# Kernel optimization log

Measured on AMD Instinct MI355X. Metric: run time of the kernel, lower is better.

## Reference

```python
import jax, jax.numpy as jnp
import numpy as np

# --- hyperparameters (from MambaBlock init) ---
DIM = 256          # d_model per window
STEP = 128         # int(dim * hop), hop = 0.5
N_MAMBA = 2
D_STATE = 16
D_CONV = 4
EXPAND = 4
D_INNER = EXPAND * DIM          # 1024
DT_RANK = -(-DIM // 16)         # ceil(d_model/16) = 16
EPS = 1e-5
B_SZ = 4
T_LEN = 131072


def setup_inputs() -> dict:
    key = jax.random.key(0)
    ks = jax.random.split(key, 8)
    s = 0.02
    x = jax.random.normal(ks[0], (B_SZ, T_LEN), dtype=jnp.float32)
    in_proj_w = jax.random.normal(ks[1], (N_MAMBA, 2 * D_INNER, DIM), dtype=jnp.float32) * s
    conv_w = jax.random.normal(ks[2], (N_MAMBA, D_INNER, 1, D_CONV), dtype=jnp.float32) * 0.1
    conv_b = jnp.zeros((N_MAMBA, D_INNER), dtype=jnp.float32)
    x_proj_w = jax.random.normal(ks[3], (N_MAMBA, DT_RANK + 2 * D_STATE, D_INNER), dtype=jnp.float32) * s
    dt_std = DT_RANK ** -0.5
    dt_proj_w = jax.random.uniform(ks[4], (N_MAMBA, D_INNER, DT_RANK), minval=-dt_std, maxval=dt_std, dtype=jnp.float32)
    # dt bias: inverse-softplus of dt ~ LogUniform[1e-3, 0.1] (mamba_ssm init)
    dt = jnp.exp(jax.random.uniform(ks[5], (N_MAMBA, D_INNER), dtype=jnp.float32)
                 * (np.log(0.1) - np.log(1e-3)) + np.log(1e-3))
    dt_proj_b = dt + jnp.log(-jnp.expm1(-dt))
    A_log = jnp.log(jnp.broadcast_to(jnp.arange(1, D_STATE + 1, dtype=jnp.float32),
                                     (N_MAMBA, D_INNER, D_STATE)))
    D_param = jnp.ones((N_MAMBA, D_INNER), dtype=jnp.float32)
    out_proj_w = jax.random.normal(ks[6], (N_MAMBA, DIM, D_INNER), dtype=jnp.float32) * s
    norm_w = jnp.ones((N_MAMBA, DIM), dtype=jnp.float32)
    return dict(x=x, in_proj_w=in_proj_w, conv_w=conv_w, conv_b=conv_b,
                x_proj_w=x_proj_w, dt_proj_w=dt_proj_w, dt_proj_b=dt_proj_b,
                A_log=A_log, D_param=D_param, out_proj_w=out_proj_w, norm_w=norm_w)


def _rmsnorm(x, w):
    return x * jax.lax.rsqrt(jnp.mean(x * x, axis=-1, keepdims=True) + EPS) * w


def _selective_scan(u, delta, A, Bm, Cm, Dp):
    # u, delta: [B, L, Di]; A: [Di, N]; Bm, Cm: [B, L, N]; Dp: [Di]
    def step(h, inp):
        u_t, d_t, B_t, C_t = inp                       # [B,Di],[B,Di],[B,N],[B,N]
        dA = jnp.exp(d_t[:, :, None] * A)              # [B,Di,N]
        h = dA * h + (d_t * u_t)[:, :, None] * B_t[:, None, :]
        y_t = jnp.einsum('bdn,bn->bd', h, C_t)
        return h, y_t
    h0 = jnp.zeros((u.shape[0], u.shape[2], A.shape[1]), u.dtype)
    xs = (u.transpose(1, 0, 2), delta.transpose(1, 0, 2),
          Bm.transpose(1, 0, 2), Cm.transpose(1, 0, 2))
    _, ys = jax.lax.scan(step, h0, xs)                 # ys: [L, B, Di]
    return ys.transpose(1, 0, 2) + u * Dp


def _mamba(x, in_w, cw, cb, xp_w, dt_w, dt_b, A_log, Dp, out_w):
    # x: [B, L, d_model]
    xz = jnp.einsum('bld,ed->ble', x, in_w)            # [B, L, 2*Di]
    xc, z = jnp.split(xz, 2, axis=-1)
    # causal depthwise conv (torch pads d_conv-1 both sides then truncates to L)
    xc = xc.transpose(0, 2, 1)                         # [B, Di, L]
    xc = jax.lax.conv_general_dilated(xc, cw, window_strides=(1,),
                                      padding=[(D_CONV - 1, 0)],
                                      feature_group_count=D_INNER,
                                      dimension_numbers=('NCH', 'OIH', 'NCH'))
    xc = jax.nn.silu(xc + cb[None, :, None]).transpose(0, 2, 1)  # [B, L, Di]
    x_dbl = jnp.einsum('bld,ed->ble', xc, xp_w)        # [B, L, dt_rank + 2N]
    dt = x_dbl[..., :DT_RANK]
    Bm = x_dbl[..., DT_RANK:DT_RANK + D_STATE]
    Cm = x_dbl[..., DT_RANK + D_STATE:]
    delta = jax.nn.softplus(jnp.einsum('blr,dr->bld', dt, dt_w) + dt_b)
    A = -jnp.exp(A_log)                                # [Di, N]
    y = _selective_scan(xc, delta, A, Bm, Cm, Dp)
    y = y * jax.nn.silu(z)
    return jnp.einsum('bld,ed->ble', y, out_w)         # [B, L, d_model]


def _forward(x, in_proj_w, conv_w, conv_b, x_proj_w, dt_proj_w, dt_proj_b,
             A_log, D_param, out_proj_w, norm_w):
    B, T = x.shape
    L = (T - DIM) // STEP + 1
    idx = jnp.arange(L)[:, None] * STEP + jnp.arange(DIM)[None, :]  # [L, DIM]
    h = x[:, idx]                                      # unfold -> [B, L, DIM]
    res = None
    for i in range(N_MAMBA):
        res = h + res if res is not None else h        # Block residual chaining
        hn = _rmsnorm(res, norm_w[i])
        h = _mamba(hn, in_proj_w[i], conv_w[i], conv_b[i], x_proj_w[i],
                   dt_proj_w[i], dt_proj_b[i], A_log[i], D_param[i], out_proj_w[i])
    r = h + res
    # hop < 1: triangular window, then fold (overlap-add)
    half = DIM // 2
    win = jnp.concatenate([jnp.linspace(0.0, 1.0, half), jnp.linspace(1.0, 0.0, half)])
    r = r * win
    folded = jnp.zeros_like(x).at[:, idx].add(r)       # F.fold overlap-add
    return folded + x


def reference(x, in_proj_w, conv_w, conv_b, x_proj_w, dt_proj_w, dt_proj_b,
              A_log, D_param, out_proj_w, norm_w):
    return _forward(x, in_proj_w, conv_w, conv_b, x_proj_w, dt_proj_w, dt_proj_b,
                    A_log, D_param, out_proj_w, norm_w)
```

## Files before the change

kernel.cpp:

```cpp
#include <hip/hip_runtime.h>
#include <cmath>

#define DIMC   256
#define L_WIN  1023
#define M_VALID 4092
#define M_PAD  4096
#define DI     1024
#define TLEN   131072
#define SEG    32
#define NSEG   32
#define CBT    8

typedef __bf16 bf16x8 __attribute__((ext_vector_type(8)));
typedef __bf16 bf16x4 __attribute__((ext_vector_type(4)));
typedef float  f32x4  __attribute__((ext_vector_type(4)));

__device__ __forceinline__ float sigmoidf_(float x){ return 1.f/(1.f + __expf(-x)); }
__device__ __forceinline__ float softplusf_(float v){ return fmaxf(v,0.f) + log1pf(__expf(-fabsf(v))); }

template<int CTRL>
__device__ __forceinline__ float dpp_add(float x){
  int v = __builtin_amdgcn_update_dpp(0, __builtin_bit_cast(int, x), CTRL, 0xF, 0xF, true);
  return x + __builtin_bit_cast(float, v);
}

__global__ __launch_bounds__(256) void init_kernel(const float* __restrict__ x, float* __restrict__ res,
    const float* __restrict__ a, __bf16* __restrict__ da, int na,
    const float* __restrict__ b, __bf16* __restrict__ db, int nb,
    const float* __restrict__ c, __bf16* __restrict__ dc, int nc)
{
  if (blockIdx.x < M_PAD){
    int m = blockIdx.x, j = threadIdx.x;
    float v = 0.f;
    if (m < M_VALID){
      int bb = m / L_WIN, l = m - bb*L_WIN;
      v = x[(size_t)bb*TLEN + l*128 + j];
    }
    res[(size_t)m*DIMC + j] = v;
    return;
  }
  int nblk = gridDim.x - M_PAD;
  int stride = nblk*256;
  int base = (blockIdx.x - M_PAD)*256 + threadIdx.x;
  for (int i = base; i < na; i += stride) da[i] = (__bf16)a[i];
  for (int i = base; i < nb; i += stride) db[i] = (__bf16)b[i];
  for (int i = base; i < nc; i += stride) dc[i] = (__bf16)c[i];
}

__global__ __launch_bounds__(256) void rms_kernel(const float* __restrict__ src, __bf16* __restrict__ dst,
                                                  const float* __restrict__ w){
  int m = blockIdx.x, j = threadIdx.x;
  float v = (m < M_VALID) ? src[(size_t)m*DIMC + j] : 0.f;
  float s = v*v;
  #pragma unroll
  for (int off = 32; off; off >>= 1) s += __shfl_down(s, off);
  __shared__ float ls[4];
  if ((threadIdx.x & 63) == 0) ls[threadIdx.x >> 6] = s;
  __syncthreads();
  float tot = ls[0] + ls[1] + ls[2] + ls[3];
  float scale = rsqrtf(tot * (1.f/DIMC) + 1e-5f);
  dst[(size_t)m*DIMC + j] = (__bf16)(v * scale * w[j]);
}

template<int WM, int WN, typename OutT>
__global__ __launch_bounds__(256) void gemm_tiled_kernel(const __bf16* __restrict__ A, const __bf16* __restrict__ B,
    OutT* C, const float* addsrc, int K, int ldc)
{
  constexpr int BM  = 32*WM;
  constexpr int BN  = 32*WN;
  constexpr int LDK = 72;
  __shared__ __bf16 As[BM*LDK];
  __shared__ __bf16 Bs[BN*LDK];
  int tid  = threadIdx.x;
  int lane = tid & 63, wv = tid >> 6;
  int row  = lane & 15, kq = lane >> 4;
  int m0 = blockIdx.x*BM, n0 = blockIdx.y*BN;
  int wmo = (wv >> 1)*(16*WM);
  int wno = (wv &  1)*(16*WN);
  f32x4 acc[WM][WN] = {};
  for (int kt = 0; kt < K; kt += 64){
    __syncthreads();
    #pragma unroll
    for (int r = 0; r < BM/32; ++r){
      int seg = r*256 + tid;
      int rw = seg >> 3, sb = seg & 7;
      *(bf16x8*)(As + rw*LDK + sb*8) = *(const bf16x8*)(A + (size_t)(m0 + rw)*K + kt + sb*8);
    }
    #pragma unroll
    for (int r = 0; r < BN/32; ++r){
      int seg = r*256 + tid;
      int rw = seg >> 3, sb = seg & 7;
      *(bf16x8*)(Bs + rw*LDK + sb*8) = *(const bf16x8*)(B + (size_t)(n0 + rw)*K + kt + sb*8);
    }
    __syncthreads();
    #pragma unroll
    for (int ks = 0; ks < 2; ++ks){
      bf16x8 af[WM], bfr[WN];
      #pragma unroll
      for (int i = 0; i < WM; ++i) af[i]  = *(const bf16x8*)(As + (wmo + i*16 + row)*LDK + ks*32 + kq*8);
      #pragma unroll
      for (int j = 0; j < WN; ++j) bfr[j] = *(const bf16x8*)(Bs + (wno + j*16 + row)*LDK + ks*32 + kq*8);
      #pragma unroll
      for (int i = 0; i < WM; ++i){
        #pragma unroll
        for (int j = 0; j < WN; ++j)
          acc[i][j] = __builtin_amdgcn_mfma_f32_16x16x32_bf16(af[i], bfr[j], acc[i][j], 0, 0, 0);
      }
    }
  }
  #pragma unroll
  for (int i = 0; i < WM; ++i){
    int cm = m0 + wmo + i*16 + kq*4;
    #pragma unroll
    for (int j = 0; j < WN; ++j){
      int cn = n0 + wno + j*16 + row;
      #pragma unroll
      for (int ii = 0; ii < 4; ++ii){
        size_t idx = (size_t)(cm + ii)*ldc + cn;
        float v = acc[i][j][ii];
        if (addsrc) v += addsrc[idx];
        C[idx] = (OutT)v;
      }
    }
  }
}

__global__ __launch_bounds__(256) void conv_xproj_dt_kernel(
  const __bf16* __restrict__ xz16, const float* __restrict__ cw, const float* __restrict__ cb,
  const __bf16* __restrict__ wxp, const float* __restrict__ dtw, const float* __restrict__ dtb,
  __bf16* __restrict__ u16, float* __restrict__ xdbl, __bf16* __restrict__ delta16)
{
  __shared__ __bf16 su[16][1032];
  __shared__ float  sdt[CBT][17];
  __shared__ f32x4  spart[4][3][64];
  int tid = threadIdx.x;
  int m0 = blockIdx.x * CBT;
  {
    int d = tid * 4;
    float w[4][4], bias[4];
    #pragma unroll
    for (int c = 0; c < 4; ++c){
      #pragma unroll
      for (int j = 0; j < 4; ++j) w[c][j] = cw[(d + c)*4 + j];
      bias[c] = cb[d + c];
    }
    bf16x4 zero4; zero4[0] = (__bf16)0.f; zero4[1] = (__bf16)0.f; zero4[2] = (__bf16)0.f; zero4[3] = (__bf16)0.f;
    bf16x4 rm3 = (m0 >= 3) ? *(const bf16x4*)(xz16 + (size_t)(m0-3)*2048 + d) : zero4;
    bf16x4 rm2 = (m0 >= 2) ? *(const bf16x4*)(xz16 + (size_t)(m0-2)*2048 + d) : zero4;
    bf16x4 rm1 = (m0 >= 1) ? *(const bf16x4*)(xz16 + (size_t)(m0-1)*2048 + d) : zero4;
    for (int ti = 0; ti < CBT; ++ti){
      int m = m0 + ti;
      bf16x4 cur = *(const bf16x4*)(xz16 + (size_t)m*2048 + d);
      float acc[4] = {0.f, 0.f, 0.f, 0.f};
      if (m < M_VALID){
        int b = m / L_WIN;
        int l = m - b*L_WIN;
        #pragma unroll
        for (int c = 0; c < 4; ++c) acc[c] = fmaf((float)cur[c], w[c][3], bias[c]);
        if (l >= 1){
          #pragma unroll
          for (int c = 0; c < 4; ++c) acc[c] = fmaf((float)rm1[c], w[c][2], acc[c]);
        }
        if (l >= 2){
          #pragma unroll
          for (int c = 0; c < 4; ++c) acc[c] = fmaf((float)rm2[c], w[c][1], acc[c]);
        }
        if (l >= 3){
          #pragma unroll
          for (int c = 0; c < 4; ++c) acc[c] = fmaf((float)rm3[c], w[c][0], acc[c]);
        }
        #pragma unroll
        for (int c = 0; c < 4; ++c) acc[c] = acc[c] * sigmoidf_(acc[c]);
      }
      bf16x4 o;
      #pragma unroll
      for (int c = 0; c < 4; ++c) o[c] = (__bf16)acc[c];
      *(bf16x4*)(u16 + (size_t)m*DI + d) = o;
      *(bf16x4*)(&su[ti][d]) = o;
      rm3 = rm2; rm2 = rm1; rm1 = cur;
    }
  }
  __syncthreads();
  {
    int lane = tid & 63, wv = tid >> 6;
    int row = lane & 15, kq = lane >> 4;
    int kbase = wv * 256;
    f32x4 acc0 = {0,0,0,0}, acc1 = {0,0,0,0}, acc2 = {0,0,0,0};
    const __bf16* B0 = wxp + (size_t)(row)*1024      + kbase + kq*8;
    const __bf16* B1 = wxp + (size_t)(16 + row)*1024 + kbase + kq*8;
    const __bf16* B2 = wxp + (size_t)(32 + row)*1024 + kbase + kq*8;
    #pragma unroll
    for (int k = 0; k < 256; k += 32){
      bf16x8 a = *(const bf16x8*)(&su[row][kbase + k + kq*8]);
      acc0 = __builtin_amdgcn_mfma_f32_16x16x32_bf16(a, *(const bf16x8*)(B0 + k), acc0, 0, 0, 0);
      acc1 = __builtin_amdgcn_mfma_f32_16x16x32_bf16(a, *(const bf16x8*)(B1 + k), acc1, 0, 0, 0);
      acc2 = __builtin_amdgcn_mfma_f32_16x16x32_bf16(a, *(const bf16x8*)(B2 + k), acc2, 0, 0, 0);
    }
    spart[wv][0][lane] = acc0;
    spart[wv][1][lane] = acc1;
    spart[wv][2][lane] = acc2;
  }
  __syncthreads();
  if (tid < 192){
    int tno = tid >> 6, lane = tid & 63;
    int row = lane & 15, kq = lane >> 4;
    f32x4 sum = spart[0][tno][lane];
    sum += spart[1][tno][lane];
    sum += spart[2][tno][lane];
    sum += spart[3][tno][lane];
    #pragma unroll
    for (int i = 0; i < 4; ++i){
      int tok = kq*4 + i;
      if (tok < CBT){
        xdbl[(size_t)(m0 + tok)*48 + tno*16 + row] = sum[i];
        if (tno == 0) sdt[tok][row] = sum[i];
      }
    }
  }
  __syncthreads();
  {
    int d0 = tid * 4;
    float w[4][16], bias[4];
    #pragma unroll
    for (int c = 0; c < 4; ++c){
      #pragma unroll
      for (int q = 0; q < 16; ++q) w[c][q] = dtw[(d0 + c)*16 + q];
      bias[c] = dtb[d0 + c];
    }
    for (int t = 0; t < CBT; ++t){
      float acc[4] = {bias[0], bias[1], bias[2], bias[3]};
      #pragma unroll
      for (int r = 0; r < 16; ++r){
        float dv = sdt[t][r];
        #pragma unroll
        for (int c = 0; c < 4; ++c) acc[c] = fmaf(dv, w[c][r], acc[c]);
      }
      bf16x4 o;
      #pragma unroll
      for (int c = 0; c < 4; ++c) o[c] = (__bf16)softplusf_(acc[c]);
      *(bf16x4*)(delta16 + (size_t)(m0 + t)*DI + d0) = o;
    }
  }
}

__global__ __launch_bounds__(256) void scan_part1_kernel(
  const __bf16* __restrict__ u16, const __bf16* __restrict__ delta16,
  const float* __restrict__ xdbl, const float* __restrict__ Alog, float2* __restrict__ Pq)
{
  int bid = blockIdx.x;
  int s = bid & 31, dtile = (bid >> 5) & 63, b = bid >> 11;
  int d0 = dtile << 4;
  int tid = threadIdx.x;
  int c = tid >> 4, n = tid & 15;
  float A_dn = -__expf(Alog[(d0 + c)*16 + n]);
  __shared__ float2 sdd[16][SEG+2];
  __shared__ float  sB [SEG][17];
  int t0 = s*SEG;
  int nt = L_WIN - t0; if (nt > SEG) nt = SEG;
  size_t base_m = (size_t)b*L_WIN + t0;
  for (int i2 = tid; i2 < 16*SEG; i2 += 256){
    int tt = i2 >> 4, dd = i2 & 15;
    float dlt = 0.f, du = 0.f, Bv = 0.f;
    if (tt < nt){
      size_t m = base_m + tt;
      dlt = (float)delta16[m*DI + d0 + dd];
      du  = dlt * (float)u16[m*DI + d0 + dd];
      Bv  = xdbl[m*48 + 16 + dd];
    }
    sdd[dd][tt] = make_float2(dlt, du);
    sB[tt][dd]  = Bv;
  }
  __syncthreads();
  float h = 0.f, P = 1.f;
  #pragma unroll 8
  for (int t = 0; t < SEG; ++t){
    float2 dd2 = sdd[c][t];
    float dA = __expf(dd2.x * A_dn);
    h = fmaf(dA, h, dd2.y * sB[t][n]);
    P *= dA;
  }
  Pq[(((size_t)b*NSEG + s) << 14) + d0*16 + tid] = make_float2(P, h);
}

__global__ __launch_bounds__(256) void scan_combine_kernel(const float2* __restrict__ Pq,
                                                           float* __restrict__ hstart)
{
  int idx = blockIdx.x*256 + threadIdx.x;
  int b = idx >> 14;
  int dn = idx & 16383;
  float hs = 0.f;
  #pragma unroll
  for (int s = 0; s < NSEG; ++s){
    size_t o = (((size_t)b*NSEG + s) << 14) + dn;
    hstart[o] = hs;
    float2 pq = Pq[o];
    hs = fmaf(pq.x, hs, pq.y);
  }
}

__global__ __launch_bounds__(256) void scan_part2_kernel(
  const __bf16* __restrict__ u16, const __bf16* __restrict__ delta16,
  const float* __restrict__ xdbl, const __bf16* __restrict__ xz16,
  const float* __restrict__ Alog, const float* __restrict__ Dp,
  const float* __restrict__ hstart, __bf16* __restrict__ y16)
{
  int bid = blockIdx.x;
  int s = bid & 31, dtile = (bid >> 5) & 63, b = bid >> 11;
  int d0 = dtile << 4;
  int tid = threadIdx.x;
  int c = tid >> 4, n = tid & 15;
  float A_dn = -__expf(Alog[(d0 + c)*16 + n]);
  __shared__ float2 sdd[16][SEG+2];
  __shared__ float2 sBC[SEG][17];
  __shared__ float  sy [16][SEG+1];
  __shared__ float  sD[16];
  if (tid < 16) sD[tid] = Dp[d0 + tid];
  int t0 = s*SEG;
  int nt = L_WIN - t0; if (nt > SEG) nt = SEG;
  size_t base_m = (size_t)b*L_WIN + t0;
  for (int i2 = tid; i2 < 16*SEG; i2 += 256){
    int tt = i2 >> 4, dd = i2 & 15;
    float dlt = 0.f, uu = 0.f, Bv = 0.f, Cv = 0.f;
    if (tt < nt){
      size_t m = base_m + tt;
      dlt = (float)delta16[m*DI + d0 + dd];
      uu  = (float)u16[m*DI + d0 + dd];
      Bv  = xdbl[m*48 + 16 + dd];
      Cv  = xdbl[m*48 + 32 + dd];
    }
    sdd[dd][tt] = make_float2(dlt, uu);
    sBC[tt][dd] = make_float2(Bv, Cv);
  }
  float h = hstart[(((size_t)b*NSEG + s) << 14) + d0*16 + tid];
  __syncthreads();
  #pragma unroll 8
  for (int t = 0; t < SEG; ++t){
    float2 dd2 = sdd[c][t];
    float dA = __expf(dd2.x * A_dn);
    float2 bc = sBC[t][n];
    h = fmaf(dA, h, dd2.x * dd2.y * bc.x);
    float pp = h * bc.y;
    pp = dpp_add<0xB1>(pp);
    pp = dpp_add<0x4E>(pp);
    pp = dpp_add<0x141>(pp);
    pp = dpp_add<0x128>(pp);
    if (n == 0) sy[c][t] = pp;
  }
  __syncthreads();
  for (int i2 = tid; i2 < 16*nt; i2 += 256){
    int tt = i2 >> 4, dd = i2 & 15;
    size_t m = base_m + tt;
    float uv = sdd[dd][tt].y;
    float zv = (float)xz16[m*2048 + 1024 + d0 + dd];
    float yv = (sy[dd][tt] + uv * sD[dd]) * (zv * sigmoidf_(zv));
    y16[m*DI + d0 + dd] = (__bf16)yv;
  }
}

__global__ __launch_bounds__(256) void fold_kernel(const float* __restrict__ x, const float* __restrict__ r,
                                                   float* __restrict__ out){
  int i = blockIdx.x*256 + threadIdx.x;
  int b = i >> 17;
  int t = i & (TLEN - 1);
  float acc = x[i];
  int l1 = t >> 7;
  int j  = t & 127;
  if (l1 < L_WIN) acc += r[((size_t)b*L_WIN + l1)*DIMC + j] * ((float)j * (1.f/127.f));
  if (l1 >= 1)    acc += r[((size_t)b*L_WIN + l1 - 1)*DIMC + j + 128] * ((float)(127 - j) * (1.f/127.f));
  out[i] = acc;
}

extern "C" void kernel_launch(void* const* d_in, const int* in_sizes, int n_in,
                              void* d_out, int out_size, void* d_ws, size_t ws_size,
                              hipStream_t stream)
{
  (void)in_sizes; (void)n_in; (void)out_size; (void)ws_size;
  const float* x      = (const float*)d_in[0];
  const float* in_w   = (const float*)d_in[1];
  const float* conv_w = (const float*)d_in[2];
  const float* conv_b = (const float*)d_in[3];
  const float* xp_w   = (const float*)d_in[4];
  const float* dt_w   = (const float*)d_in[5];
  const float* dt_b   = (const float*)d_in[6];
  const float* A_log  = (const float*)d_in[7];
  const float* Dp     = (const float*)d_in[8];
  const float* out_w  = (const float*)d_in[9];
  const float* norm_w = (const float*)d_in[10];
  float* out = (float*)d_out;

  char* p = (char*)d_ws;
  auto alloc = [&](size_t bytes)->void*{ void* r = (void*)p; p += (bytes + 255) & ~(size_t)255; return r; };
  float*  res    = (float*) alloc((size_t)M_PAD*DIMC*4);
  __bf16* hn16   = (__bf16*)alloc((size_t)M_PAD*DIMC*2);
  __bf16* xz16   = (__bf16*)alloc((size_t)M_PAD*2048*2);
  __bf16* u16    = (__bf16*)alloc((size_t)M_PAD*DI*2);
  float*  xdbl   = (float*) alloc((size_t)M_PAD*48*4);
  __bf16* delta16= (__bf16*)alloc((size_t)M_PAD*DI*2);
  __bf16* y16    = (__bf16*)alloc((size_t)M_PAD*DI*2);
  float2* Pq     = (float2*)alloc((size_t)4*NSEG*16384*8);
  float*  hstart = (float*) alloc((size_t)4*NSEG*16384*4);
  __bf16* w_in16 = (__bf16*)alloc((size_t)2*2048*256*2);
  __bf16* w_xp16 = (__bf16*)alloc((size_t)2*48*1024*2);
  __bf16* w_out16= (__bf16*)alloc((size_t)2*256*1024*2);

  init_kernel<<<M_PAD + 512, 256, 0, stream>>>(x, res,
                                               in_w, w_in16, 2*2048*256,
                                               xp_w, w_xp16, 2*48*1024,
                                               out_w, w_out16, 2*256*1024);

  for (int i = 0; i < 2; ++i){
    rms_kernel<<<M_PAD, 256, 0, stream>>>(res, hn16, norm_w + i*256);
    gemm_tiled_kernel<4, 4, __bf16><<<dim3(32, 16), 256, 0, stream>>>(hn16, w_in16 + (size_t)i*524288, xz16, nullptr, 256, 2048);
    conv_xproj_dt_kernel<<<M_PAD/CBT, 256, 0, stream>>>(xz16, conv_w + i*4096, conv_b + i*1024,
                                                        w_xp16 + (size_t)i*49152, dt_w + i*16384, dt_b + i*1024,
                                                        u16, xdbl, delta16);
    scan_part1_kernel<<<8192, 256, 0, stream>>>(u16, delta16, xdbl, A_log + i*16384, Pq);
    scan_combine_kernel<<<256, 256, 0, stream>>>(Pq, hstart);
    scan_part2_kernel<<<8192, 256, 0, stream>>>(u16, delta16, xdbl, xz16, A_log + i*16384, Dp + i*1024,
                                                hstart, y16);
    gemm_tiled_kernel<2, 2, float><<<dim3(64, 4), 256, 0, stream>>>(y16, w_out16 + (size_t)i*262144, res, res, 1024, 256);
  }
  fold_kernel<<<TLEN*4/256, 256, 0, stream>>>(x, res, out);
}
```

Measured before the change: 327.3 us.

## Replace chunked three-kernel scan with single sequential scan; fuse RMSNorm into in-proj GEMM

The segmented scan (part1, combine, part2 over 8192 blocks) becomes one kernel of 256 blocks. Each block walks all 1023 timesteps for a batch and 16-channel tile, double-buffering 64-token chunks through shared memory. The RMSNorm now runs inside the input projection GEMM, which computes per-row scales and normalizes while staging A tiles. This removes the Pq/hstart traffic, the repeated input loads and the extra launches, but it cuts scan parallelism to 256 blocks of long serial loops on a GPU with many CUs.

```diff
diff --git a/kernel.cpp b/kernel.cpp
--- a/kernel.cpp
+++ b/kernel.cpp
@@ -7,9 +7,9 @@
 #define M_PAD  4096
 #define DI     1024
 #define TLEN   131072
-#define SEG    32
-#define NSEG   32
 #define CBT    8
+#define CH     64
+#define NCH    16
 
 typedef __bf16 bf16x8 __attribute__((ext_vector_type(8)));
 typedef __bf16 bf16x4 __attribute__((ext_vector_type(4)));
@@ -47,19 +47,92 @@
   for (int i = base; i < nc; i += stride) dc[i] = (__bf16)c[i];
 }
 
-__global__ __launch_bounds__(256) void rms_kernel(const float* __restrict__ src, __bf16* __restrict__ dst,
-                                                  const float* __restrict__ w){
-  int m = blockIdx.x, j = threadIdx.x;
-  float v = (m < M_VALID) ? src[(size_t)m*DIMC + j] : 0.f;
-  float s = v*v;
+template<int WM, int WN>
+__global__ __launch_bounds__(256) void gemm_rms_kernel(const float* __restrict__ Araw,
+    const __bf16* __restrict__ B, const float* __restrict__ wn, __bf16* __restrict__ C, int ldc)
+{
+  constexpr int BM  = 32*WM;
+  constexpr int BN  = 32*WN;
+  constexpr int LDK = 72;
+  __shared__ __bf16 As[BM*LDK];
+  __shared__ __bf16 Bs[BN*LDK];
+  __shared__ float  sscale[BM];
+  __shared__ float  swn[256];
+  int tid  = threadIdx.x;
+  int lane = tid & 63, wv = tid >> 6;
+  int row  = lane & 15, kq = lane >> 4;
+  int m0 = blockIdx.x*BM, n0 = blockIdx.y*BN;
+  int wmo = (wv >> 1)*(16*WM);
+  int wno = (wv &  1)*(16*WN);
+  {
+    swn[tid] = wn[tid];
+    int r = tid >> 1, half = tid & 1;
+    int gr = m0 + r;
+    float s = 0.f;
+    if (gr < M_VALID){
+      const f32x4* src = (const f32x4*)(Araw + (size_t)gr*DIMC + half*128);
+      #pragma unroll
+      for (int i = 0; i < 32; ++i){
+        f32x4 v = src[i];
+        s += v[0]*v[0] + v[1]*v[1] + v[2]*v[2] + v[3]*v[3];
+      }
+    }
+    s += __shfl_xor(s, 1);
+    if (half == 0) sscale[r] = (gr < M_VALID) ? rsqrtf(s*(1.f/DIMC) + 1e-5f) : 0.f;
+  }
+  f32x4 acc[WM][WN] = {};
+  for (int kt = 0; kt < 256; kt += 64){
+    __syncthreads();
+    #pragma unroll
+    for (int r2 = 0; r2 < BM/32; ++r2){
+      int seg = r2*256 + tid;
+      int rw = seg >> 3, sb = seg & 7;
+      int gr = m0 + rw;
+      float sc = sscale[rw];
+      const float* ap = Araw + (size_t)gr*DIMC + kt + sb*8;
+      f32x4 v0 = {0,0,0,0}, v1 = {0,0,0,0};
+      if (gr < M_VALID){ v0 = *(const f32x4*)ap; v1 = *(const f32x4*)(ap + 4); }
+      bf16x8 o;
+      #pragma unroll
+      for (int j = 0; j < 4; ++j){
+        o[j]   = (__bf16)(v0[j] * sc * swn[kt + sb*8 + j]);
+        o[4+j] = (__bf16)(v1[j] * sc * swn[kt + sb*8 + 4 + j]);
+      }
+      *(bf16x8*)(As + rw*LDK + sb*8) = o;
+    }
+    #pragma unroll
+    for (int r2 = 0; r2 < BN/32; ++r2){
+      int seg = r2*256 + tid;
+      int rw = seg >> 3, sb = seg & 7;
+      *(bf16x8*)(Bs + rw*LDK + sb*8) = *(const bf16x8*)(B + (size_t)(n0 + rw)*256 + kt + sb*8);
+    }
+    __syncthreads();
+    #pragma unroll
+    for (int ks = 0; ks < 2; ++ks){
+      bf16x8 af[WM], bfr[WN];
+      #pragma unroll
+      for (int i = 0; i < WM; ++i) af[i]  = *(const bf16x8*)(As + (wmo + i*16 + row)*LDK + ks*32 + kq*8);
+      #pragma unroll
+      for (int j = 0; j < WN; ++j) bfr[j] = *(const bf16x8*)(Bs + (wno + j*16 + row)*LDK + ks*32 + kq*8);
+      #pragma unroll
+      for (int i = 0; i < WM; ++i){
+        #pragma unroll
+        for (int j = 0; j < WN; ++j)
+          acc[i][j] = __builtin_amdgcn_mfma_f32_16x16x32_bf16(af[i], bfr[j], acc[i][j], 0, 0, 0);
+      }
+    }
+  }
   #pragma unroll
-  for (int off = 32; off; off >>= 1) s += __shfl_down(s, off);
-  __shared__ float ls[4];
-  if ((threadIdx.x & 63) == 0) ls[threadIdx.x >> 6] = s;
-  __syncthreads();
-  float tot = ls[0] + ls[1] + ls[2] + ls[3];
-  float scale = rsqrtf(tot * (1.f/DIMC) + 1e-5f);
-  dst[(size_t)m*DIMC + j] = (__bf16)(v * scale * w[j]);
+  for (int i = 0; i < WM; ++i){
+    int cm = m0 + wmo + i*16 + kq*4;
+    #pragma unroll
+    for (int j = 0; j < WN; ++j){
+      int cn = n0 + wno + j*16 + row;
+      #pragma unroll
+      for (int ii = 0; ii < 4; ++ii)
+        C[(size_t)(cm + ii)*ldc + cn] = (__bf16)acc[i][j][ii];
+    }
+  }
 }
 
 template<int WM, int WN, typename OutT>
@@ -243,117 +316,106 @@
   }
 }
 
-__global__ __launch_bounds__(256) void scan_part1_kernel(
+__global__ __launch_bounds__(256) void scan_full_kernel(
   const __bf16* __restrict__ u16, const __bf16* __restrict__ delta16,
-  const float* __restrict__ xdbl, const float* __restrict__ Alog, float2* __restrict__ Pq)
+  const float* __restrict__ xdbl, const __bf16* __restrict__ xz16,
+  const float* __restrict__ Alog, const float* __restrict__ Dp,
+  __bf16* __restrict__ y16)
 {
   int bid = blockIdx.x;
-  int s = bid & 31, dtile = (bid >> 5) & 63, b = bid >> 11;
+  int o = (bid & 7)*32 + (bid >> 3);
+  int b = o >> 6, dtile = o & 63;
   int d0 = dtile << 4;
   int tid = threadIdx.x;
   int c = tid >> 4, n = tid & 15;
-  float A_dn = -__expf(Alog[(d0 + c)*16 + n]);
-  __shared__ float2 sdd[16][SEG+2];
-  __shared__ float  sB [SEG][17];
-  int t0 = s*SEG;
-  int nt = L_WIN - t0; if (nt > SEG) nt = SEG;
-  size_t base_m = (size_t)b*L_WIN + t0;
-  for (int i2 = tid; i2 < 16*SEG; i2 += 256){
-    int tt = i2 >> 4, dd = i2 & 15;
-    float dlt = 0.f, du = 0.f, Bv = 0.f;
-    if (tt < nt){
-      size_t m = base_m + tt;
-      dlt = (float)delta16[m*DI + d0 + dd];
-      du  = dlt * (float)u16[m*DI + d0 + dd];
-      Bv  = xdbl[m*48 + 16 + dd];
-    }
-    sdd[dd][tt] = make_float2(dlt, du);
-    sB[tt][dd]  = Bv;
-  }
+  float A2 = -__expf(Alog[(d0 + c)*16 + n]) * 1.4426950408889634f;
+
+  __shared__ float2 sdu[2][CH][16];
+  __shared__ float2 sBC[2][CH][16];
+  __shared__ __bf16 su [2][CH][16];
+  __shared__ __bf16 sz [2][CH][16];
+  __shared__ float  sy [CH][16];
+
+  size_t brow = (size_t)b * L_WIN;
+  int tt = tid >> 2;
+  int q  = (tid & 3) << 2;
+
+  float rD[4];
+  #pragma unroll
+  for (int j = 0; j < 4; ++j) rD[j] = Dp[d0 + q + j];
+
+  bf16x4 r_dl, r_uu, r_zz; f32x4 r_B, r_C;
+  bf16x4 zero4; zero4[0] = (__bf16)0.f; zero4[1] = (__bf16)0.f; zero4[2] = (__bf16)0.f; zero4[3] = (__bf16)0.f;
+
+  auto LOAD = [&](int k){
+    int tok = k*CH + tt;
+    if (tok < L_WIN){
+      size_t m = brow + tok;
+      r_dl = *(const bf16x4*)(delta16 + m*DI + d0 + q);
+      r_uu = *(const bf16x4*)(u16    + m*DI + d0 + q);
+      r_zz = *(const bf16x4*)(xz16   + m*2048 + 1024 + d0 + q);
+      r_B  = *(const f32x4*)(xdbl + m*48 + 16 + q);
+      r_C  = *(const f32x4*)(xdbl + m*48 + 32 + q);
+    } else {
+      r_dl = zero4; r_uu = zero4; r_zz = zero4;
+      r_B = f32x4{0,0,0,0}; r_C = f32x4{0,0,0,0};
+    }
+  };
+  auto WRITE = [&](int bf){
+    #pragma unroll
+    for (int j = 0; j < 4; ++j){
+      float dlt = (float)r_dl[j], uu = (float)r_uu[j];
+      sdu[bf][tt][q + j] = make_float2(dlt, dlt*uu);
+      sBC[bf][tt][q + j] = make_float2(r_B[j], r_C[j]);
+    }
+    *(bf16x4*)(&su[bf][tt][q]) = r_uu;
+    *(bf16x4*)(&sz[bf][tt][q]) = r_zz;
+  };
+
+  LOAD(0);
+  WRITE(0);
+  LOAD(1);
   __syncthreads();
-  float h = 0.f, P = 1.f;
-  #pragma unroll 8
-  for (int t = 0; t < SEG; ++t){
-    float2 dd2 = sdd[c][t];
-    float dA = __expf(dd2.x * A_dn);
-    h = fmaf(dA, h, dd2.y * sB[t][n]);
-    P *= dA;
-  }
-  Pq[(((size_t)b*NSEG + s) << 14) + d0*16 + tid] = make_float2(P, h);
-}
-
-__global__ __launch_bounds__(256) void scan_combine_kernel(const float2* __restrict__ Pq,
-                                                           float* __restrict__ hstart)
-{
-  int idx = blockIdx.x*256 + threadIdx.x;
-  int b = idx >> 14;
-  int dn = idx & 16383;
-  float hs = 0.f;
-  #pragma unroll
-  for (int s = 0; s < NSEG; ++s){
-    size_t o = (((size_t)b*NSEG + s) << 14) + dn;
-    hstart[o] = hs;
-    float2 pq = Pq[o];
-    hs = fmaf(pq.x, hs, pq.y);
-  }
-}
-
-__global__ __launch_bounds__(256) void scan_part2_kernel(
-  const __bf16* __restrict__ u16, const __bf16* __restrict__ delta16,
-  const float* __restrict__ xdbl, const __bf16* __restrict__ xz16,
-  const float* __restrict__ Alog, const float* __restrict__ Dp,
-  const float* __restrict__ hstart, __bf16* __restrict__ y16)
-{
-  int bid = blockIdx.x;
-  int s = bid & 31, dtile = (bid >> 5) & 63, b = bid >> 11;
-  int d0 = dtile << 4;
-  int tid = threadIdx.x;
-  int c = tid >> 4, n = tid & 15;
-  float A_dn = -__expf(Alog[(d0 + c)*16 + n]);
-  __shared__ float2 sdd[16][SEG+2];
-  __shared__ float2 sBC[SEG][17];
-  __shared__ float  sy [16][SEG+1];
-  __shared__ float  sD[16];
-  if (tid < 16) sD[tid] = Dp[d0 + tid];
-  int t0 = s*SEG;
-  int nt = L_WIN - t0; if (nt > SEG) nt = SEG;
-  size_t base_m = (size_t)b*L_WIN + t0;
-  for (int i2 = tid; i2 < 16*SEG; i2 += 256){
-    int tt = i2 >> 4, dd = i2 & 15;
-    float dlt = 0.f, uu = 0.f, Bv = 0.f, Cv = 0.f;
-    if (tt < nt){
-      size_t m = base_m + tt;
-      dlt = (float)delta16[m*DI + d0 + dd];
-      uu  = (float)u16[m*DI + d0 + dd];
-      Bv  = xdbl[m*48 + 16 + dd];
-      Cv  = xdbl[m*48 + 32 + dd];
-    }
-    sdd[dd][tt] = make_float2(dlt, uu);
-    sBC[tt][dd] = make_float2(Bv, Cv);
-  }
-  float h = hstart[(((size_t)b*NSEG + s) << 14) + d0*16 + tid];
-  __syncthreads();
-  #pragma unroll 8
-  for (int t = 0; t < SEG; ++t){
-    float2 dd2 = sdd[c][t];
-    float dA = __expf(dd2.x * A_dn);
-    float2 bc = sBC[t][n];
-    h = fmaf(dA, h, dd2.x * dd2.y * bc.x);
-    float pp = h * bc.y;
-    pp = dpp_add<0xB1>(pp);
-    pp = dpp_add<0x4E>(pp);
-    pp = dpp_add<0x141>(pp);
-    pp = dpp_add<0x128>(pp);
-    if (n == 0) sy[c][t] = pp;
-  }
-  __syncthreads();
-  for (int i2 = tid; i2 < 16*nt; i2 += 256){
-    int tt = i2 >> 4, dd = i2 & 15;
-    size_t m = base_m + tt;
-    float uv = sdd[dd][tt].y;
-    float zv = (float)xz16[m*2048 + 1024 + d0 + dd];
-    float yv = (sy[dd][tt] + uv * sD[dd]) * (zv * sigmoidf_(zv));
-    y16[m*DI + d0 + dd] = (__bf16)yv;
+
+  float h = 0.f;
+  for (int k = 0; k < NCH; ++k){
+    int bf = k & 1;
+    #pragma unroll 8
+    for (int t = 0; t < CH; ++t){
+      float2 du = sdu[bf][t][c];
+      float dA = exp2f(du.x * A2);
+      float2 bc = sBC[bf][t][n];
+      h = fmaf(dA, h, du.y * bc.x);
+      float pp = h * bc.y;
+      pp = dpp_add<0xB1>(pp);
+      pp = dpp_add<0x4E>(pp);
+      pp = dpp_add<0x141>(pp);
+      pp = dpp_add<0x128>(pp);
+      if (n == 0) sy[t][c] = pp;
+    }
+    __syncthreads();
+    if (k + 1 < NCH){
+      WRITE(bf ^ 1);
+      if (k + 2 < NCH) LOAD(k + 2);
+    }
+    {
+      int tok = k*CH + tt;
+      if (tok < L_WIN){
+        size_t m = brow + tok;
+        f32x4  yv = *(const f32x4*)(&sy[tt][q]);
+        bf16x4 u4 = *(const bf16x4*)(&su[bf][tt][q]);
+        bf16x4 z4 = *(const bf16x4*)(&sz[bf][tt][q]);
+        bf16x4 ov;
+        #pragma unroll
+        for (int j = 0; j < 4; ++j){
+          float zf = (float)z4[j];
+          float y  = (yv[j] + (float)u4[j]*rD[j]) * (zf * sigmoidf_(zf));
+          ov[j] = (__bf16)y;
+        }
+        *(bf16x4*)(y16 + m*DI + d0 + q) = ov;
+      }
+    }
+    __syncthreads();
   }
 }
 
@@ -391,14 +453,11 @@
   char* p = (char*)d_ws;
   auto alloc = [&](size_t bytes)->void*{ void* r = (void*)p; p += (bytes + 255) & ~(size_t)255; return r; };
   float*  res    = (float*) alloc((size_t)M_PAD*DIMC*4);
-  __bf16* hn16   = (__bf16*)alloc((size_t)M_PAD*DIMC*2);
   __bf16* xz16   = (__bf16*)alloc((size_t)M_PAD*2048*2);
   __bf16* u16    = (__bf16*)alloc((size_t)M_PAD*DI*2);
   float*  xdbl   = (float*) alloc((size_t)M_PAD*48*4);
   __bf16* delta16= (__bf16*)alloc((size_t)M_PAD*DI*2);
   __bf16* y16    = (__bf16*)alloc((size_t)M_PAD*DI*2);
-  float2* Pq     = (float2*)alloc((size_t)4*NSEG*16384*8);
-  float*  hstart = (float*) alloc((size_t)4*NSEG*16384*4);
   __bf16* w_in16 = (__bf16*)alloc((size_t)2*2048*256*2);
   __bf16* w_xp16 = (__bf16*)alloc((size_t)2*48*1024*2);
   __bf16* w_out16= (__bf16*)alloc((size_t)2*256*1024*2);
@@ -409,15 +468,13 @@
                                                out_w, w_out16, 2*256*1024);
 
   for (int i = 0; i < 2; ++i){
-    rms_kernel<<<M_PAD, 256, 0, stream>>>(res, hn16, norm_w + i*256);
-    gemm_tiled_kernel<4, 4, __bf16><<<dim3(32, 16), 256, 0, stream>>>(hn16, w_in16 + (size_t)i*524288, xz16, nullptr, 256, 2048);
+    gemm_rms_kernel<4, 4><<<dim3(32, 16), 256, 0, stream>>>(res, w_in16 + (size_t)i*524288,
+                                                            norm_w + i*256, xz16, 2048);
     conv_xproj_dt_kernel<<<M_PAD/CBT, 256, 0, stream>>>(xz16, conv_w + i*4096, conv_b + i*1024,
                                                         w_xp16 + (size_t)i*49152, dt_w + i*16384, dt_b + i*1024,
                                                         u16, xdbl, delta16);
-    scan_part1_kernel<<<8192, 256, 0, stream>>>(u16, delta16, xdbl, A_log + i*16384, Pq);
-    scan_combine_kernel<<<256, 256, 0, stream>>>(Pq, hstart);
-    scan_part2_kernel<<<8192, 256, 0, stream>>>(u16, delta16, xdbl, xz16, A_log + i*16384, Dp + i*1024,
-                                                hstart, y16);
+    scan_full_kernel<<<256, 256, 0, stream>>>(u16, delta16, xdbl, xz16,
+                                              A_log + i*16384, Dp + i*1024, y16);
     gemm_tiled_kernel<2, 2, float><<<dim3(64, 4), 256, 0, stream>>>(y16, w_out16 + (size_t)i*262144, res, res, 1024, 256);
   }
   fold_kernel<<<TLEN*4/256, 256, 0, stream>>>(x, res, out);
```

Measured after the change: 458.6 us. 1.4x slower.

## Fuse RMSNorm into in_proj GEMM and use exp2 in scan kernels

Applied to the files above, without the earlier changes.

Removes the separate RMSNorm kernel and its bf16 intermediate buffer. The in_proj GEMM now computes per-row RMS scales itself and applies scale and norm weight while staging fp32 activations into shared memory as bf16. Each of the 16 column blocks recomputes the row norms and reads fp32 input twice, trading extra redundant reads for one fewer launch and round trip. The scan kernels also fold log2e into A so they can call exp2f instead of __expf.

```diff
diff --git a/kernel.cpp b/kernel.cpp
--- a/kernel.cpp
+++ b/kernel.cpp
@@ -15,6 +15,8 @@
 typedef __bf16 bf16x4 __attribute__((ext_vector_type(4)));
 typedef float  f32x4  __attribute__((ext_vector_type(4)));
 
+#define LOG2E 1.4426950408889634f
+
 __device__ __forceinline__ float sigmoidf_(float x){ return 1.f/(1.f + __expf(-x)); }
 __device__ __forceinline__ float softplusf_(float v){ return fmaxf(v,0.f) + log1pf(__expf(-fabsf(v))); }
 
@@ -47,19 +49,92 @@
   for (int i = base; i < nc; i += stride) dc[i] = (__bf16)c[i];
 }
 
-__global__ __launch_bounds__(256) void rms_kernel(const float* __restrict__ src, __bf16* __restrict__ dst,
-                                                  const float* __restrict__ w){
-  int m = blockIdx.x, j = threadIdx.x;
-  float v = (m < M_VALID) ? src[(size_t)m*DIMC + j] : 0.f;
-  float s = v*v;
+template<int WM, int WN>
+__global__ __launch_bounds__(256) void gemm_rms_kernel(const float* __restrict__ Araw,
+    const __bf16* __restrict__ B, const float* __restrict__ wn, __bf16* __restrict__ C, int ldc)
+{
+  constexpr int BM  = 32*WM;
+  constexpr int BN  = 32*WN;
+  constexpr int LDK = 72;
+  __shared__ __bf16 As[BM*LDK];
+  __shared__ __bf16 Bs[BN*LDK];
+  __shared__ float  sscale[BM];
+  __shared__ float  swn[256];
+  int tid  = threadIdx.x;
+  int lane = tid & 63, wv = tid >> 6;
+  int row  = lane & 15, kq = lane >> 4;
+  int m0 = blockIdx.x*BM, n0 = blockIdx.y*BN;
+  int wmo = (wv >> 1)*(16*WM);
+  int wno = (wv &  1)*(16*WN);
+  {
+    swn[tid] = wn[tid];
+    int r = tid >> 1, half = tid & 1;
+    int gr = m0 + r;
+    float s = 0.f;
+    if (gr < M_VALID){
+      const f32x4* src = (const f32x4*)(Araw + (size_t)gr*DIMC + half*128);
+      #pragma unroll
+      for (int i = 0; i < 32; ++i){
+        f32x4 v = src[i];
+        s += v[0]*v[0] + v[1]*v[1] + v[2]*v[2] + v[3]*v[3];
+      }
+    }
+    s += __shfl_xor(s, 1);
+    if (half == 0) sscale[r] = (gr < M_VALID) ? rsqrtf(s*(1.f/DIMC) + 1e-5f) : 0.f;
+  }
+  f32x4 acc[WM][WN] = {};
+  for (int kt = 0; kt < 256; kt += 64){
+    __syncthreads();
+    #pragma unroll
+    for (int r2 = 0; r2 < BM/32; ++r2){
+      int seg = r2*256 + tid;
+      int rw = seg >> 3, sb = seg & 7;
+      int gr = m0 + rw;
+      float sc = sscale[rw];
+      const float* ap = Araw + (size_t)gr*DIMC + kt + sb*8;
+      f32x4 v0 = {0,0,0,0}, v1 = {0,0,0,0};
+      if (gr < M_VALID){ v0 = *(const f32x4*)ap; v1 = *(const f32x4*)(ap + 4); }
+      bf16x8 o;
+      #pragma unroll
+      for (int j = 0; j < 4; ++j){
+        o[j]   = (__bf16)(v0[j] * sc * swn[kt + sb*8 + j]);
+        o[4+j] = (__bf16)(v1[j] * sc * swn[kt + sb*8 + 4 + j]);
+      }
+      *(bf16x8*)(As + rw*LDK + sb*8) = o;
+    }
+    #pragma unroll
+    for (int r2 = 0; r2 < BN/32; ++r2){
+      int seg = r2*256 + tid;
+      int rw = seg >> 3, sb = seg & 7;
+      *(bf16x8*)(Bs + rw*LDK + sb*8) = *(const bf16x8*)(B + (size_t)(n0 + rw)*256 + kt + sb*8);
+    }
+    __syncthreads();
+    #pragma unroll
+    for (int ks = 0; ks < 2; ++ks){
+      bf16x8 af[WM], bfr[WN];
+      #pragma unroll
+      for (int i = 0; i < WM; ++i) af[i]  = *(const bf16x8*)(As + (wmo + i*16 + row)*LDK + ks*32 + kq*8);
+      #pragma unroll
+      for (int j = 0; j < WN; ++j) bfr[j] = *(const bf16x8*)(Bs + (wno + j*16 + row)*LDK + ks*32 + kq*8);
+      #pragma unroll
+      for (int i = 0; i < WM; ++i){
+        #pragma unroll
+        for (int j = 0; j < WN; ++j)
+          acc[i][j] = __builtin_amdgcn_mfma_f32_16x16x32_bf16(af[i], bfr[j], acc[i][j], 0, 0, 0);
+      }
+    }
+  }
   #pragma unroll
-  for (int off = 32; off; off >>= 1) s += __shfl_down(s, off);
-  __shared__ float ls[4];
-  if ((threadIdx.x & 63) == 0) ls[threadIdx.x >> 6] = s;
-  __syncthreads();
-  float tot = ls[0] + ls[1] + ls[2] + ls[3];
-  float scale = rsqrtf(tot * (1.f/DIMC) + 1e-5f);
-  dst[(size_t)m*DIMC + j] = (__bf16)(v * scale * w[j]);
+  for (int i = 0; i < WM; ++i){
+    int cm = m0 + wmo + i*16 + kq*4;
+    #pragma unroll
+    for (int j = 0; j < WN; ++j){
+      int cn = n0 + wno + j*16 + row;
+      #pragma unroll
+      for (int ii = 0; ii < 4; ++ii)
+        C[(size_t)(cm + ii)*ldc + cn] = (__bf16)acc[i][j][ii];
+    }
+  }
 }
 
 template<int WM, int WN, typename OutT>
@@ -252,7 +327,7 @@
   int d0 = dtile << 4;
   int tid = threadIdx.x;
   int c = tid >> 4, n = tid & 15;
-  float A_dn = -__expf(Alog[(d0 + c)*16 + n]);
+  float A2 = -__expf(Alog[(d0 + c)*16 + n]) * LOG2E;
   __shared__ float2 sdd[16][SEG+2];
   __shared__ float  sB [SEG][17];
   int t0 = s*SEG;
@@ -275,7 +350,7 @@
   #pragma unroll 8
   for (int t = 0; t < SEG; ++t){
     float2 dd2 = sdd[c][t];
-    float dA = __expf(dd2.x * A_dn);
+    float dA = exp2f(dd2.x * A2);
     h = fmaf(dA, h, dd2.y * sB[t][n]);
     P *= dA;
   }
@@ -309,7 +384,7 @@
   int d0 = dtile << 4;
   int tid = threadIdx.x;
   int c = tid >> 4, n = tid & 15;
-  float A_dn = -__expf(Alog[(d0 + c)*16 + n]);
+  float A2 = -__expf(Alog[(d0 + c)*16 + n]) * LOG2E;
   __shared__ float2 sdd[16][SEG+2];
   __shared__ float2 sBC[SEG][17];
   __shared__ float  sy [16][SEG+1];
@@ -336,7 +411,7 @@
   #pragma unroll 8
   for (int t = 0; t < SEG; ++t){
     float2 dd2 = sdd[c][t];
-    float dA = __expf(dd2.x * A_dn);
+    float dA = exp2f(dd2.x * A2);
     float2 bc = sBC[t][n];
     h = fmaf(dA, h, dd2.x * dd2.y * bc.x);
     float pp = h * bc.y;
@@ -391,7 +466,6 @@
   char* p = (char*)d_ws;
   auto alloc = [&](size_t bytes)->void*{ void* r = (void*)p; p += (bytes + 255) & ~(size_t)255; return r; };
   float*  res    = (float*) alloc((size_t)M_PAD*DIMC*4);
-  __bf16* hn16   = (__bf16*)alloc((size_t)M_PAD*DIMC*2);
   __bf16* xz16   = (__bf16*)alloc((size_t)M_PAD*2048*2);
   __bf16* u16    = (__bf16*)alloc((size_t)M_PAD*DI*2);
   float*  xdbl   = (float*) alloc((size_t)M_PAD*48*4);
@@ -409,8 +483,8 @@
                                                out_w, w_out16, 2*256*1024);
 
   for (int i = 0; i < 2; ++i){
-    rms_kernel<<<M_PAD, 256, 0, stream>>>(res, hn16, norm_w + i*256);
-    gemm_tiled_kernel<4, 4, __bf16><<<dim3(32, 16), 256, 0, stream>>>(hn16, w_in16 + (size_t)i*524288, xz16, nullptr, 256, 2048);
+    gemm_rms_kernel<4, 4><<<dim3(32, 16), 256, 0, stream>>>(res, w_in16 + (size_t)i*524288,
+                                                            norm_w + i*256, xz16, 2048);
     conv_xproj_dt_kernel<<<M_PAD/CBT, 256, 0, stream>>>(xz16, conv_w + i*4096, conv_b + i*1024,
                                                         w_xp16 + (size_t)i*49152, dt_w + i*16384, dt_b + i*1024,
                                                         u16, xdbl, delta16);
```

New measurement: 354.3 us. 8.3% more time.

## Fold scan combine into part2, compute segment decay via summed delta, retile GEMMs

Applied to the files above, without the earlier changes.

Removes the separate scan_combine kernel and the hstart buffer. Each part2 block now rebuilds its starting state by serially combining the prefix (P,h) pairs of the earlier segments. The segment decay product is computed as a single exp2 of the summed delta instead of a running product. Segments are doubled to 64 steps so there are half as many, and both GEMMs use smaller tiles along one dimension to launch more blocks. The trade-off is redundant prefix work in part2, a longer serial loop per block, and fewer scan blocks.

```diff
diff --git a/kernel.cpp b/kernel.cpp
--- a/kernel.cpp
+++ b/kernel.cpp
@@ -7,13 +7,15 @@
 #define M_PAD  4096
 #define DI     1024
 #define TLEN   131072
-#define SEG    32
-#define NSEG   32
+#define SEG    64
+#define NSEG   16
 #define CBT    8
 
 typedef __bf16 bf16x8 __attribute__((ext_vector_type(8)));
 typedef __bf16 bf16x4 __attribute__((ext_vector_type(4)));
 typedef float  f32x4  __attribute__((ext_vector_type(4)));
+
+#define LOG2E 1.4426950408889634f
 
 __device__ __forceinline__ float sigmoidf_(float x){ return 1.f/(1.f + __expf(-x)); }
 __device__ __forceinline__ float softplusf_(float v){ return fmaxf(v,0.f) + log1pf(__expf(-fabsf(v))); }
@@ -248,11 +250,11 @@
   const float* __restrict__ xdbl, const float* __restrict__ Alog, float2* __restrict__ Pq)
 {
   int bid = blockIdx.x;
-  int s = bid & 31, dtile = (bid >> 5) & 63, b = bid >> 11;
+  int s = bid & 15, dtile = (bid >> 4) & 63, b = bid >> 10;
   int d0 = dtile << 4;
   int tid = threadIdx.x;
   int c = tid >> 4, n = tid & 15;
-  float A_dn = -__expf(Alog[(d0 + c)*16 + n]);
+  float A2 = -__expf(Alog[(d0 + c)*16 + n]) * LOG2E;
   __shared__ float2 sdd[16][SEG+2];
   __shared__ float  sB [SEG][17];
   int t0 = s*SEG;
@@ -271,50 +273,40 @@
     sB[tt][dd]  = Bv;
   }
   __syncthreads();
-  float h = 0.f, P = 1.f;
+  float h = 0.f, sd = 0.f;
   #pragma unroll 8
   for (int t = 0; t < SEG; ++t){
     float2 dd2 = sdd[c][t];
-    float dA = __expf(dd2.x * A_dn);
+    float dA = exp2f(dd2.x * A2);
     h = fmaf(dA, h, dd2.y * sB[t][n]);
-    P *= dA;
-  }
-  Pq[(((size_t)b*NSEG + s) << 14) + d0*16 + tid] = make_float2(P, h);
-}
-
-__global__ __launch_bounds__(256) void scan_combine_kernel(const float2* __restrict__ Pq,
-                                                           float* __restrict__ hstart)
-{
-  int idx = blockIdx.x*256 + threadIdx.x;
-  int b = idx >> 14;
-  int dn = idx & 16383;
-  float hs = 0.f;
-  #pragma unroll
-  for (int s = 0; s < NSEG; ++s){
-    size_t o = (((size_t)b*NSEG + s) << 14) + dn;
-    hstart[o] = hs;
-    float2 pq = Pq[o];
-    hs = fmaf(pq.x, hs, pq.y);
-  }
+    sd += dd2.x;
+  }
+  float P = exp2f(sd * A2);
+  Pq[(((size_t)b*NSEG + s) << 14) + (dtile << 8) + tid] = make_float2(P, h);
 }
 
 __global__ __launch_bounds__(256) void scan_part2_kernel(
   const __bf16* __restrict__ u16, const __bf16* __restrict__ delta16,
   const float* __restrict__ xdbl, const __bf16* __restrict__ xz16,
   const float* __restrict__ Alog, const float* __restrict__ Dp,
-  const float* __restrict__ hstart, __bf16* __restrict__ y16)
+  const float2* __restrict__ Pq, __bf16* __restrict__ y16)
 {
   int bid = blockIdx.x;
-  int s = bid & 31, dtile = (bid >> 5) & 63, b = bid >> 11;
+  int s = bid & 15, dtile = (bid >> 4) & 63, b = bid >> 10;
   int d0 = dtile << 4;
   int tid = threadIdx.x;
   int c = tid >> 4, n = tid & 15;
-  float A_dn = -__expf(Alog[(d0 + c)*16 + n]);
+  float A2 = -__expf(Alog[(d0 + c)*16 + n]) * LOG2E;
   __shared__ float2 sdd[16][SEG+2];
   __shared__ float2 sBC[SEG][17];
   __shared__ float  sy [16][SEG+1];
   __shared__ float  sD[16];
   if (tid < 16) sD[tid] = Dp[d0 + tid];
+  float h = 0.f;
+  for (int sp = 0; sp < s; ++sp){
+    float2 pq = Pq[(((size_t)b*NSEG + sp) << 14) + (dtile << 8) + tid];
+    h = fmaf(pq.x, h, pq.y);
+  }
   int t0 = s*SEG;
   int nt = L_WIN - t0; if (nt > SEG) nt = SEG;
   size_t base_m = (size_t)b*L_WIN + t0;
@@ -331,12 +323,11 @@
     sdd[dd][tt] = make_float2(dlt, uu);
     sBC[tt][dd] = make_float2(Bv, Cv);
   }
-  float h = hstart[(((size_t)b*NSEG + s) << 14) + d0*16 + tid];
   __syncthreads();
   #pragma unroll 8
   for (int t = 0; t < SEG; ++t){
     float2 dd2 = sdd[c][t];
-    float dA = __expf(dd2.x * A_dn);
+    float dA = exp2f(dd2.x * A2);
     float2 bc = sBC[t][n];
     h = fmaf(dA, h, dd2.x * dd2.y * bc.x);
     float pp = h * bc.y;
@@ -398,7 +389,6 @@
   __bf16* delta16= (__bf16*)alloc((size_t)M_PAD*DI*2);
   __bf16* y16    = (__bf16*)alloc((size_t)M_PAD*DI*2);
   float2* Pq     = (float2*)alloc((size_t)4*NSEG*16384*8);
-  float*  hstart = (float*) alloc((size_t)4*NSEG*16384*4);
   __bf16* w_in16 = (__bf16*)alloc((size_t)2*2048*256*2);
   __bf16* w_xp16 = (__bf16*)alloc((size_t)2*48*1024*2);
   __bf16* w_out16= (__bf16*)alloc((size_t)2*256*1024*2);
@@ -410,15 +400,14 @@
 
   for (int i = 0; i < 2; ++i){
     rms_kernel<<<M_PAD, 256, 0, stream>>>(res, hn16, norm_w + i*256);
-    gemm_tiled_kernel<4, 4, __bf16><<<dim3(32, 16), 256, 0, stream>>>(hn16, w_in16 + (size_t)i*524288, xz16, nullptr, 256, 2048);
+    gemm_tiled_kernel<4, 2, __bf16><<<dim3(32, 32), 256, 0, stream>>>(hn16, w_in16 + (size_t)i*524288, xz16, nullptr, 256, 2048);
     conv_xproj_dt_kernel<<<M_PAD/CBT, 256, 0, stream>>>(xz16, conv_w + i*4096, conv_b + i*1024,
                                                         w_xp16 + (size_t)i*49152, dt_w + i*16384, dt_b + i*1024,
                                                         u16, xdbl, delta16);
-    scan_part1_kernel<<<8192, 256, 0, stream>>>(u16, delta16, xdbl, A_log + i*16384, Pq);
-    scan_combine_kernel<<<256, 256, 0, stream>>>(Pq, hstart);
-    scan_part2_kernel<<<8192, 256, 0, stream>>>(u16, delta16, xdbl, xz16, A_log + i*16384, Dp + i*1024,
-                                                hstart, y16);
-    gemm_tiled_kernel<2, 2, float><<<dim3(64, 4), 256, 0, stream>>>(y16, w_out16 + (size_t)i*262144, res, res, 1024, 256);
+    scan_part1_kernel<<<4096, 256, 0, stream>>>(u16, delta16, xdbl, A_log + i*16384, Pq);
+    scan_part2_kernel<<<4096, 256, 0, stream>>>(u16, delta16, xdbl, xz16, A_log + i*16384, Dp + i*1024,
+                                                Pq, y16);
+    gemm_tiled_kernel<2, 1, float><<<dim3(64, 8), 256, 0, stream>>>(y16, w_out16 + (size_t)i*262144, res, res, 1024, 256);
   }
   fold_kernel<<<TLEN*4/256, 256, 0, stream>>>(x, res, out);
 }
```

Measured after the change: 325.2 us. About the same (-0.7%).
